# Optimization experiments

Measured on AMD Instinct MI355X. Metric: run time of the kernel, lower is better.

The kernel has to match this reference:

```python
import jax, jax.numpy as jnp
import numpy as np

B, C, H, W = 2, 64, 192, 192
K = 3
KK = K * K  # 9 kernel taps


def conv2d(x, w, b, dilation=1, padding=1):
    # NCHW / OIHW 3x3 conv, stride 1
    out = jax.lax.conv_general_dilated(
        x, w, window_strides=(1, 1),
        padding=[(padding, padding), (padding, padding)],
        rhs_dilation=(dilation, dilation),
        dimension_numbers=('NCHW', 'OIHW', 'NCHW'))
    return out + b[None, :, None, None]


def channel_ln(x, w, b, eps=1e-5):
    # WithBias_LayerNorm over the channel axis (to_3d puts C last)
    mu = jnp.mean(x, axis=1, keepdims=True)
    var = jnp.mean((x - mu) ** 2, axis=1, keepdims=True)  # biased var
    xn = (x - mu) / jnp.sqrt(var + eps)
    return xn * w[None, :, None, None] + b[None, :, None, None]


def mod_deform_conv(x, offset, mask, w, b):
    # Modulated deformable conv (mmcv semantics): stride 1, pad 1, dil 1,
    # deform_groups=1. offset: [B,2*KK,H,W] (dy,dx interleaved per tap),
    # mask: [B,KK,H,W].
    Bb, Cc, Hh, Ww = x.shape
    off = offset.reshape(Bb, KK, 2, Hh, Ww)
    kidx = jnp.arange(K)
    ky, kx = jnp.meshgrid(kidx, kidx, indexing='ij')
    ky = ky.reshape(KK).astype(x.dtype)
    kx = kx.reshape(KK).astype(x.dtype)
    hh = jnp.arange(Hh, dtype=x.dtype)
    ww = jnp.arange(Ww, dtype=x.dtype)
    # sample positions: out_pos - pad + tap + learned offset  -> [B,KK,H,W]
    py = off[:, :, 0] + hh[None, None, :, None] - 1.0 + ky[None, :, None, None]
    px = off[:, :, 1] + ww[None, None, None, :] - 1.0 + kx[None, :, None, None]
    y0f = jnp.floor(py)
    x0f = jnp.floor(px)
    ly = py - y0f
    lx = px - x0f
    y0 = y0f.astype(jnp.int32)
    x0 = x0f.astype(jnp.int32)
    xf = x.reshape(Bb, Cc, Hh * Ww)

    def corner(yi, xi, wgt):
        valid = (yi >= 0) & (yi < Hh) & (xi >= 0) & (xi < Ww)
        idx = (jnp.clip(yi, 0, Hh - 1) * Ww + jnp.clip(xi, 0, Ww - 1)).reshape(Bb, -1)
        g = jax.vmap(lambda xb, ib: xb[:, ib])(xf, idx)  # [B,C,KK*H*W]
        wv = (wgt * valid.astype(x.dtype)).reshape(Bb, 1, -1)
        return g * wv

    val = (corner(y0, x0, (1 - ly) * (1 - lx))
           + corner(y0, x0 + 1, (1 - ly) * lx)
           + corner(y0 + 1, x0, ly * (1 - lx))
           + corner(y0 + 1, x0 + 1, ly * lx))
    val = val.reshape(Bb, Cc, KK, Hh, Ww) * mask[:, None]  # modulate
    out = jnp.einsum('bckhw,ock->bohw', val, w.reshape(w.shape[0], Cc, KK))
    return out + b[None, :, None, None]


def setup_inputs() -> dict:
    key = jax.random.key(0)
    ks = jax.random.split(key, 8)
    x = jax.random.normal(ks[0], (B, C, H, W), jnp.float32)
    pre_mask = jax.random.uniform(ks[1], (B, 1, H, W), jnp.float32)
    ln_w = jnp.ones((C,), jnp.float32)
    ln_b = jnp.zeros((C,), jnp.float32)
    # offset/mask convs are zero-init in the original; use small random
    # weights so the bilinear gather is actually exercised (offsets ~ few px)
    off_w = jax.random.normal(ks[2], (2 * KK, C, 3, 3), jnp.float32) * 0.02
    off_b = jnp.zeros((2 * KK,), jnp.float32)
    mask_w = jax.random.normal(ks[3], (KK, C, 3, 3), jnp.float32) * 0.02
    mask_b = jnp.zeros((KK,), jnp.float32)
    scale = 1.0 / np.sqrt(C * KK)
    def_w = jax.random.normal(ks[4], (C, C, 3, 3), jnp.float32) * scale
    def_b = jnp.zeros((C,), jnp.float32)
    fus_w = jax.random.normal(ks[5], (C, C, 3, 3), jnp.float32) * scale
    fus_b = jnp.zeros((C,), jnp.float32)
    return {'x': x, 'pre_mask': pre_mask, 'ln_w': ln_w, 'ln_b': ln_b,
            'off_w': off_w, 'off_b': off_b, 'mask_w': mask_w, 'mask_b': mask_b,
            'def_w': def_w, 'def_b': def_b, 'fus_w': fus_w, 'fus_b': fus_b}


def reference(x, pre_mask, ln_w, ln_b, off_w, off_b, mask_w, mask_b,
              def_w, def_b, fus_w, fus_b):
    inp = x
    xn = channel_ln(x, ln_w, ln_b)
    # only the dilation=1 offset/mask branch feeds the single def_conv
    offset = conv2d(xn, off_w, off_b, dilation=1, padding=1)
    mask = jax.nn.sigmoid(conv2d(xn, mask_w, mask_b, dilation=1, padding=1))
    x_def = mod_deform_conv(xn, offset, mask, def_w, def_b)
    # single def_conv -> stack+sum is identity
    return conv2d(x_def, fus_w, fus_b) * pre_mask + inp * (1.0 - pre_mask)
```

## Files before the change

### kernel.cpp

```cpp
#include <hip/hip_runtime.h>
#include <hip/hip_bf16.h>
#include <math.h>

#define B_ 2
#define C_ 64
#define H_ 192
#define W_ 192
#define HW_ (H_*W_)
#define BHW_ (B_*HW_)
#define KK_ 9
#define CK_ (C_*KK_)
#define KSTEPS_ (CK_/32)
#define TX_ 12
#define WROWS_ 6
#define WCOLS_ 21
#define WCHUNKS_ (WROWS_*WCOLS_*8)
#define FWROWS_ 4
#define FWCOLS_ 18
#define FWCHUNKS_ (FWROWS_*FWCOLS_*8)

typedef __bf16 bf16x8 __attribute__((ext_vector_type(8)));
typedef float  f32x4  __attribute__((ext_vector_type(4)));
typedef unsigned short ushortx8 __attribute__((ext_vector_type(8)));
typedef unsigned short ushortx4 __attribute__((ext_vector_type(4)));

__device__ __forceinline__ float bf2f(unsigned short u) {
    unsigned int t = ((unsigned int)u) << 16;
    return __builtin_bit_cast(float, t);
}
__device__ __forceinline__ unsigned short f2bf(float f) {
    __hip_bfloat16 hb = __float2bfloat16(f);
    return *reinterpret_cast<unsigned short*>(&hb);
}

__global__ void ln_prepack_kernel(const float* __restrict__ x,
                                  const float* __restrict__ lnw,
                                  const float* __restrict__ lnb,
                                  unsigned short* __restrict__ xnb,
                                  const float* __restrict__ dw,
                                  const float* __restrict__ fw,
                                  const float* __restrict__ offw,
                                  const float* __restrict__ maskw,
                                  unsigned short* __restrict__ wpack,
                                  unsigned short* __restrict__ wpf,
                                  unsigned short* __restrict__ wpc) {
    if (blockIdx.x < 288) {
        int p = blockIdx.x * 256 + threadIdx.x;
        int b = p / HW_, pix = p % HW_;
        const float* xb = x + (size_t)b * C_ * HW_ + pix;
        float v[C_];
        float s = 0.f, s2 = 0.f;
        #pragma unroll
        for (int c = 0; c < C_; ++c) {
            v[c] = xb[(size_t)c * HW_];
            s += v[c]; s2 += v[c] * v[c];
        }
        float mu  = s * (1.0f / C_);
        float var = s2 * (1.0f / C_) - mu * mu;
        float inv = rsqrtf(var + 1e-5f);
        unsigned short* zb = xnb + (size_t)p * 64;
        #pragma unroll
        for (int g = 0; g < 8; ++g) {
            ushortx8 st;
            #pragma unroll
            for (int j = 0; j < 8; ++j) {
                int c = g * 8 + j;
                st[j] = f2bf((v[c] - mu) * inv * lnw[c] + lnb[c]);
            }
            *reinterpret_cast<ushortx8*>(zb + g * 8) = st;
        }
        return;
    }
    const int n1 = 4 * KSTEPS_ * 64 * 8;
    const int n2 = 4 * KSTEPS_ * 64 * 8;
    const int n3 = 2 * KSTEPS_ * 64 * 8;
    int gid = (blockIdx.x - 288) * 256 + threadIdx.x;
    int nth = 36 * 256;
    for (int idx = gid; idx < n1 + n2 + n3; idx += nth) {
        int which = (idx < n1) ? 0 : (idx < n1 + n2 ? 1 : 2);
        int rem = idx - (which == 0 ? 0 : (which == 1 ? n1 : n1 + n2));
        int j = rem & 7;
        int l = (rem >> 3) & 63;
        int rest = rem >> 9;
        int s = rest % KSTEPS_;
        int t = rest / KSTEPS_;
        int oc = t * 16 + (l & 15);
        int ck = s * 32 + (l >> 4) * 8 + j;
        int k = ck >> 6, c = ck & 63;
        float v;
        if (which == 0) {
            v = dw[(size_t)oc * CK_ + c * 9 + k];
        } else if (which == 1) {
            v = fw[(size_t)oc * CK_ + c * 9 + k];
        } else {
            v = (oc < 18) ? offw[(size_t)oc * CK_ + c * 9 + k]
              : (oc < 27) ? maskw[(size_t)(oc - 18) * CK_ + c * 9 + k]
              : 0.f;
        }
        unsigned short u = f2bf(v);
        if (which == 0) wpack[rem] = u;
        else if (which == 1) wpf[rem] = u;
        else wpc[rem] = u;
    }
}

__global__ void __launch_bounds__(128) dc_mfma(
        const unsigned short* __restrict__ xnb,
        const unsigned short* __restrict__ wpc,
        const float* __restrict__ offb, const float* __restrict__ maskb,
        const unsigned short* __restrict__ wpack,
        const float* __restrict__ db,
        unsigned short* __restrict__ xdefb) {
    __shared__ ushortx8 win[WCHUNKS_];
    __shared__ float som[32][36];
    int tid  = threadIdx.x;
    int wave = tid >> 6;
    int lane = tid & 63;
    int bid  = blockIdx.x;
    int rg   = bid % (H_ / 2);
    int rest = bid / (H_ / 2);
    int tx   = rest % TX_;
    int b    = rest / TX_;
    int pq = lane & 15;
    int kchunk = lane >> 4;
    int h0 = rg * 2;
    int w0 = tx * 16, w = w0 + pq;

    const unsigned short* xb = xnb + (size_t)b * HW_ * 64;

    #pragma unroll
    for (int i = 0; i < 8; ++i) {
        int idx = i * 128 + tid;
        if (idx < WCHUNKS_) {
            int r    = idx / (WCOLS_ * 8);
            int rem2 = idx - r * (WCOLS_ * 8);
            int c    = rem2 >> 3;
            int seg  = rem2 & 7;
            int gy = min(max(h0 - 2 + r, 0), H_ - 1);
            int gx = min(max(w0 - 2 + c, 0), W_ - 1);
            ushortx8 v = *reinterpret_cast<const ushortx8*>(
                xb + ((size_t)(gy * W_ + gx) * 64 + seg * 8));
            win[(r * WCOLS_ + c) * 8 + (seg ^ (c & 7))] = v;
        }
    }
    __syncthreads();

    f32x4 cacc[2][2];
    #pragma unroll
    for (int pg = 0; pg < 2; ++pg)
        #pragma unroll
        for (int t = 0; t < 2; ++t) cacc[pg][t] = f32x4{0.f, 0.f, 0.f, 0.f};

    #pragma unroll
    for (int s = 0; s < KSTEPS_; ++s) {
        const int k = s >> 1;
        const int dy = k / 3 - 1, dxk = k % 3 - 1;
        int wc = pq + dxk + 2;
        int sidx = ((s & 1) * 4 + kchunk) ^ (wc & 7);
        bf16x8 af[2];
        #pragma unroll
        for (int t = 0; t < 2; ++t)
            af[t] = *reinterpret_cast<const bf16x8*>(
                wpc + ((size_t)(t * KSTEPS_ + s) * 64 + lane) * 8);
        #pragma unroll
        for (int pg = 0; pg < 2; ++pg) {
            int hp = h0 + pg;
            bool ok = ((unsigned)(hp + dy) < (unsigned)H_) &&
                      ((unsigned)(w + dxk) < (unsigned)W_);
            int wr = pg + dy + 2;
            ushortx8 u = win[(wr * WCOLS_ + wc) * 8 + sidx];
            if (!ok) u = ushortx8{0, 0, 0, 0, 0, 0, 0, 0};
            bf16x8 bv = __builtin_bit_cast(bf16x8, u);
            #pragma unroll
            for (int t = 0; t < 2; ++t)
                cacc[pg][t] = __builtin_amdgcn_mfma_f32_16x16x32_bf16(af[t], bv, cacc[pg][t], 0, 0, 0);
        }
    }

    #pragma unroll
    for (int pg = 0; pg < 2; ++pg) {
        #pragma unroll
        for (int t = 0; t < 2; ++t) {
            f32x4 sv;
            #pragma unroll
            for (int r = 0; r < 4; ++r) {
                int oc = t * 16 + kchunk * 4 + r;
                float a = cacc[pg][t][r];
                if (oc < 18)      sv[r] = a + offb[oc];
                else if (oc < 27) sv[r] = 1.f / (1.f + expf(-(a + maskb[oc - 18])));
                else              sv[r] = 0.f;
            }
            *reinterpret_cast<f32x4*>(&som[pg * 16 + pq][t * 16 + kchunk * 4]) = sv;
        }
    }

    f32x4 acc[2][4];
    #pragma unroll
    for (int pg = 0; pg < 2; ++pg)
        #pragma unroll
        for (int t = 0; t < 4; ++t) acc[pg][t] = f32x4{0.f, 0.f, 0.f, 0.f};

    auto tapbody = [&](int k) {
        #pragma unroll
        for (int pg = 0; pg < 2; ++pg) {
            int hp = h0 + pg;
            const float* om = som[pg * 16 + pq];
            float dy = om[2 * k], dx = om[2 * k + 1], m = om[18 + k];
            float py = dy + (float)(hp - 1 + k / 3);
            float px = dx + (float)(w - 1 + k % 3);
            float fy = floorf(py), fx = floorf(px);
            float ly = py - fy, lx = px - fx;
            int y0 = (int)fy, x0 = (int)fx;
            int y1 = y0 + 1, x1 = x0 + 1;
            bool oky0 = (unsigned)y0 < (unsigned)H_;
            bool oky1 = (unsigned)y1 < (unsigned)H_;
            bool okx0 = (unsigned)x0 < (unsigned)W_;
            bool okx1 = (unsigned)x1 < (unsigned)W_;
            float q[4];
            q[0] = (oky0 && okx0) ? (1.f - ly) * (1.f - lx) * m : 0.f;
            q[1] = (oky0 && okx1) ? (1.f - ly) * lx * m : 0.f;
            q[2] = (oky1 && okx0) ? ly * (1.f - lx) * m : 0.f;
            q[3] = (oky1 && okx1) ? ly * lx * m : 0.f;
            int wr0 = y0 - (h0 - 2), wr1 = y1 - (h0 - 2);
            int wc0 = x0 - (w0 - 2), wc1 = x1 - (w0 - 2);
            bool inr0 = (unsigned)wr0 < (unsigned)WROWS_;
            bool inr1 = (unsigned)wr1 < (unsigned)WROWS_;
            bool inc0 = (unsigned)wc0 < (unsigned)WCOLS_;
            bool inc1 = (unsigned)wc1 < (unsigned)WCOLS_;
            bool in[4];
            in[0] = inr0 && inc0; in[1] = inr0 && inc1;
            in[2] = inr1 && inc0; in[3] = inr1 && inc1;
            int swr0 = min(max(wr0, 0), WROWS_ - 1), swr1 = min(max(wr1, 0), WROWS_ - 1);
            int swc0 = min(max(wc0, 0), WCOLS_ - 1), swc1 = min(max(wc1, 0), WCOLS_ - 1);
            int cb[4], sx[4];
            cb[0] = (swr0 * WCOLS_ + swc0) * 8; sx[0] = swc0 & 7;
            cb[1] = (swr0 * WCOLS_ + swc1) * 8; sx[1] = swc1 & 7;
            cb[2] = (swr1 * WCOLS_ + swc0) * 8; sx[2] = swc0 & 7;
            cb[3] = (swr1 * WCOLS_ + swc1) * 8; sx[3] = swc1 & 7;
            int cy0 = min(max(y0, 0), H_ - 1), cy1 = min(max(y1, 0), H_ - 1);
            int cx0 = min(max(x0, 0), W_ - 1), cx1 = min(max(x1, 0), W_ - 1);
            int ga[4];
            ga[0] = cy0 * W_ + cx0; ga[1] = cy0 * W_ + cx1;
            ga[2] = cy1 * W_ + cx0; ga[3] = cy1 * W_ + cx1;

            #pragma unroll
            for (int half = 0; half < 2; ++half) {
                int s = k * 2 + half;
                int seg = half * 4 + kchunk;
                int cbg = half * 32 + kchunk * 8;
                ushortx8 v[4];
                #pragma unroll
                for (int c = 0; c < 4; ++c) v[c] = win[cb[c] + (seg ^ sx[c])];
                #pragma unroll
                for (int c = 0; c < 4; ++c)
                    if (q[c] != 0.f && !in[c])
                        v[c] = *reinterpret_cast<const ushortx8*>(
                            xb + ((size_t)ga[c] * 64 + cbg));
                union { unsigned short u[8]; bf16x8 v; } bu;
                #pragma unroll
                for (int j = 0; j < 8; ++j) {
                    float a = q[0] * bf2f(v[0][j]) + q[1] * bf2f(v[1][j])
                            + q[2] * bf2f(v[2][j]) + q[3] * bf2f(v[3][j]);
                    bu.u[j] = f2bf(a);
                }
                #pragma unroll
                for (int t = 0; t < 4; ++t) {
                    bf16x8 afr = *reinterpret_cast<const bf16x8*>(
                        wpack + ((size_t)(t * KSTEPS_ + s) * 64 + lane) * 8);
                    acc[pg][t] = __builtin_amdgcn_mfma_f32_16x16x32_bf16(
                        afr, bu.v, acc[pg][t], 0, 0, 0);
                }
            }
        }
    };

    if (wave == 0) {
        tapbody(0); tapbody(1); tapbody(2); tapbody(3);
    } else {
        tapbody(4); tapbody(5); tapbody(6); tapbody(7); tapbody(8);
    }

    __syncthreads();
    float* red = reinterpret_cast<float*>(win);
    {
        float* slot = red + (wave * 64 + lane) * 17;
        if (wave == 0) {
            #pragma unroll
            for (int t = 0; t < 4; ++t)
                #pragma unroll
                for (int r = 0; r < 4; ++r) slot[t * 4 + r] = acc[1][t][r];
        } else {
            #pragma unroll
            for (int t = 0; t < 4; ++t)
                #pragma unroll
                for (int r = 0; r < 4; ++r) slot[t * 4 + r] = acc[0][t][r];
        }
    }
    __syncthreads();
    {
        const float* pslot = red + ((1 - wave) * 64 + lane) * 17;
        int hp = h0 + wave;
        unsigned short* zb = xdefb + ((size_t)(b * HW_ + hp * W_ + w)) * 64;
        if (wave == 0) {
            #pragma unroll
            for (int t = 0; t < 4; ++t) {
                ushortx4 st;
                #pragma unroll
                for (int r = 0; r < 4; ++r) {
                    int oc = t * 16 + kchunk * 4 + r;
                    st[r] = f2bf(acc[0][t][r] + pslot[t * 4 + r] + db[oc]);
                }
                *reinterpret_cast<ushortx4*>(zb + t * 16 + kchunk * 4) = st;
            }
        } else {
            #pragma unroll
            for (int t = 0; t < 4; ++t) {
                ushortx4 st;
                #pragma unroll
                for (int r = 0; r < 4; ++r) {
                    int oc = t * 16 + kchunk * 4 + r;
                    st[r] = f2bf(acc[1][t][r] + pslot[t * 4 + r] + db[oc]);
                }
                *reinterpret_cast<ushortx4*>(zb + t * 16 + kchunk * 4) = st;
            }
        }
    }
}

__global__ void __launch_bounds__(128) fuse_mfma(
        const unsigned short* __restrict__ xdefb,
        const unsigned short* __restrict__ wpf,
        const float* __restrict__ fb,
        const float* __restrict__ premask,
        const float* __restrict__ xin,
        float* __restrict__ out) {
    __shared__ ushortx8 fwin[FWCHUNKS_];
    int tid  = threadIdx.x;
    int wave = tid >> 6;
    int lane = tid & 63;
    int bid  = blockIdx.x;
    int rg   = bid % (H_ / 2);
    int rest = bid / (H_ / 2);
    int tx   = rest % TX_;
    int b    = rest / TX_;
    int pq = lane & 15;
    int kchunk = lane >> 4;
    int h0 = rg * 2;
    int w0 = tx * 16, w = w0 + pq;

    const unsigned short* xb = xdefb + (size_t)b * HW_ * 64;

    #pragma unroll
    for (int i = 0; i < 5; ++i) {
        int idx = i * 128 + tid;
        if (idx < FWCHUNKS_) {
            int r    = idx / (FWCOLS_ * 8);
            int rem2 = idx - r * (FWCOLS_ * 8);
            int c    = rem2 >> 3;
            int seg  = rem2 & 7;
            int gy = min(max(h0 - 1 + r, 0), H_ - 1);
            int gx = min(max(w0 - 1 + c, 0), W_ - 1);
            ushortx8 v = *reinterpret_cast<const ushortx8*>(
                xb + ((size_t)(gy * W_ + gx) * 64 + seg * 8));
            fwin[(r * FWCOLS_ + c) * 8 + (seg ^ (c & 7))] = v;
        }
    }
    __syncthreads();

    f32x4 acc[2][4];
    #pragma unroll
    for (int pg = 0; pg < 2; ++pg)
        #pragma unroll
        for (int t = 0; t < 4; ++t) acc[pg][t] = f32x4{0.f, 0.f, 0.f, 0.f};

    auto stepbody = [&](int s) {
        const int k = s >> 1;
        const int dy = k / 3 - 1, dxk = k % 3 - 1;
        int wc = pq + dxk + 1;
        int sidx = ((s & 1) * 4 + kchunk) ^ (wc & 7);
        bf16x8 af[4];
        #pragma unroll
        for (int t = 0; t < 4; ++t)
            af[t] = *reinterpret_cast<const bf16x8*>(
                wpf + ((size_t)(t * KSTEPS_ + s) * 64 + lane) * 8);
        #pragma unroll
        for (int pg = 0; pg < 2; ++pg) {
            int hp = h0 + pg;
            bool ok = ((unsigned)(hp + dy) < (unsigned)H_) &&
                      ((unsigned)(w + dxk) < (unsigned)W_);
            int wr = pg + dy + 1;
            ushortx8 u = fwin[(wr * FWCOLS_ + wc) * 8 + sidx];
            if (!ok) u = ushortx8{0, 0, 0, 0, 0, 0, 0, 0};
            bf16x8 bv = __builtin_bit_cast(bf16x8, u);
            #pragma unroll
            for (int t = 0; t < 4; ++t)
                acc[pg][t] = __builtin_amdgcn_mfma_f32_16x16x32_bf16(af[t], bv, acc[pg][t], 0, 0, 0);
        }
    };

    if (wave == 0) {
        stepbody(0); stepbody(1); stepbody(2); stepbody(3); stepbody(4);
        stepbody(5); stepbody(6); stepbody(7); stepbody(8);
    } else {
        stepbody(9); stepbody(10); stepbody(11); stepbody(12); stepbody(13);
        stepbody(14); stepbody(15); stepbody(16); stepbody(17);
    }

    __syncthreads();
    float* red = reinterpret_cast<float*>(fwin);
    {
        float* slot = red + (wave * 64 + lane) * 17;
        if (wave == 0) {
            #pragma unroll
            for (int t = 0; t < 4; ++t)
                #pragma unroll
                for (int r = 0; r < 4; ++r) slot[t * 4 + r] = acc[1][t][r];
        } else {
            #pragma unroll
            for (int t = 0; t < 4; ++t)
                #pragma unroll
                for (int r = 0; r < 4; ++r) slot[t * 4 + r] = acc[0][t][r];
        }
    }
    __syncthreads();
    {
        const float* pslot = red + ((1 - wave) * 64 + lane) * 17;
        int hp = h0 + wave;
        int pix = hp * W_ + w;
        float pm = premask[(size_t)b * HW_ + pix];
        if (wave == 0) {
            #pragma unroll
            for (int t = 0; t < 4; ++t) {
                #pragma unroll
                for (int r = 0; r < 4; ++r) {
                    int oc = t * 16 + kchunk * 4 + r;
                    size_t oidx = ((size_t)b * C_ + oc) * HW_ + pix;
                    float a = acc[0][t][r] + pslot[t * 4 + r] + fb[oc];
                    out[oidx] = a * pm + xin[oidx] * (1.f - pm);
                }
            }
        } else {
            #pragma unroll
            for (int t = 0; t < 4; ++t) {
                #pragma unroll
                for (int r = 0; r < 4; ++r) {
                    int oc = t * 16 + kchunk * 4 + r;
                    size_t oidx = ((size_t)b * C_ + oc) * HW_ + pix;
                    float a = acc[1][t][r] + pslot[t * 4 + r] + fb[oc];
                    out[oidx] = a * pm + xin[oidx] * (1.f - pm);
                }
            }
        }
    }
}

extern "C" void kernel_launch(void* const* d_in, const int* in_sizes, int n_in,
                              void* d_out, int out_size, void* d_ws, size_t ws_size,
                              hipStream_t stream) {
    const float* x       = (const float*)d_in[0];
    const float* premask = (const float*)d_in[1];
    const float* lnw     = (const float*)d_in[2];
    const float* lnb     = (const float*)d_in[3];
    const float* offw    = (const float*)d_in[4];
    const float* offb    = (const float*)d_in[5];
    const float* maskw   = (const float*)d_in[6];
    const float* maskb   = (const float*)d_in[7];
    const float* dw      = (const float*)d_in[8];
    const float* db      = (const float*)d_in[9];
    const float* fw      = (const float*)d_in[10];
    const float* fb      = (const float*)d_in[11];
    float* out = (float*)d_out;

    char* ws = (char*)d_ws;
    unsigned short* xnb   = (unsigned short*)ws;  ws += sizeof(short) * (size_t)BHW_ * 64;
    unsigned short* xdefb = (unsigned short*)ws;  ws += sizeof(short) * (size_t)BHW_ * 64;
    unsigned short* wpack = (unsigned short*)ws;  ws += sizeof(short) * 4 * KSTEPS_ * 64 * 8;
    unsigned short* wpf   = (unsigned short*)ws;  ws += sizeof(short) * 4 * KSTEPS_ * 64 * 8;
    unsigned short* wpc   = (unsigned short*)ws;  ws += sizeof(short) * 2 * KSTEPS_ * 64 * 8;

    const int grid = B_ * TX_ * (H_ / 2);

    ln_prepack_kernel<<<288 + 36, 256, 0, stream>>>(
        x, lnw, lnb, xnb, dw, fw, offw, maskw, wpack, wpf, wpc);
    dc_mfma<<<grid, 128, 0, stream>>>(
        xnb, wpc, offb, maskb, wpack, db, xdefb);
    fuse_mfma<<<grid, 128, 0, stream>>>(xdefb, wpf, fb, premask, x, out);
}
```

Baseline: 74.97 us.

## Split offset conv rows across waves and software-pipeline deform tap gathers

The offset/mask conv stage is now split so each of the two waves computes one output row instead of both waves computing both rows redundantly, followed by a barrier before the deform stage reads the shared offset table. The deform tap loop is restructured into prep (coordinate math plus LDS/global corner loads) and blend (bilinear mix plus MFMA) phases, double-buffered so the next tap's loads are issued before the current tap's math. This is meant to hide LDS and global gather latency and remove duplicated MFMA work, at the cost of more live registers (two sets of eight vector buffers) and an extra block barrier.

```diff
diff --git a/kernel.cpp b/kernel.cpp
--- a/kernel.cpp
+++ b/kernel.cpp
@@ -145,54 +145,45 @@
     }
     __syncthreads();
 
-    f32x4 cacc[2][2];
-    #pragma unroll
-    for (int pg = 0; pg < 2; ++pg)
-        #pragma unroll
-        for (int t = 0; t < 2; ++t) cacc[pg][t] = f32x4{0.f, 0.f, 0.f, 0.f};
-
-    #pragma unroll
-    for (int s = 0; s < KSTEPS_; ++s) {
-        const int k = s >> 1;
-        const int dy = k / 3 - 1, dxk = k % 3 - 1;
-        int wc = pq + dxk + 2;
-        int sidx = ((s & 1) * 4 + kchunk) ^ (wc & 7);
-        bf16x8 af[2];
-        #pragma unroll
-        for (int t = 0; t < 2; ++t)
-            af[t] = *reinterpret_cast<const bf16x8*>(
-                wpc + ((size_t)(t * KSTEPS_ + s) * 64 + lane) * 8);
-        #pragma unroll
-        for (int pg = 0; pg < 2; ++pg) {
-            int hp = h0 + pg;
+    {
+        int hp = h0 + wave;
+        f32x4 cacc[2];
+        cacc[0] = f32x4{0.f, 0.f, 0.f, 0.f};
+        cacc[1] = f32x4{0.f, 0.f, 0.f, 0.f};
+        #pragma unroll
+        for (int s = 0; s < KSTEPS_; ++s) {
+            const int k = s >> 1;
+            const int dy = k / 3 - 1, dxk = k % 3 - 1;
+            int wc = pq + dxk + 2;
+            int sidx = ((s & 1) * 4 + kchunk) ^ (wc & 7);
             bool ok = ((unsigned)(hp + dy) < (unsigned)H_) &&
                       ((unsigned)(w + dxk) < (unsigned)W_);
-            int wr = pg + dy + 2;
+            int wr = wave + dy + 2;
             ushortx8 u = win[(wr * WCOLS_ + wc) * 8 + sidx];
             if (!ok) u = ushortx8{0, 0, 0, 0, 0, 0, 0, 0};
             bf16x8 bv = __builtin_bit_cast(bf16x8, u);
             #pragma unroll
-            for (int t = 0; t < 2; ++t)
-                cacc[pg][t] = __builtin_amdgcn_mfma_f32_16x16x32_bf16(af[t], bv, cacc[pg][t], 0, 0, 0);
-        }
-    }
-
-    #pragma unroll
-    for (int pg = 0; pg < 2; ++pg) {
+            for (int t = 0; t < 2; ++t) {
+                bf16x8 afrag = *reinterpret_cast<const bf16x8*>(
+                    wpc + ((size_t)(t * KSTEPS_ + s) * 64 + lane) * 8);
+                cacc[t] = __builtin_amdgcn_mfma_f32_16x16x32_bf16(afrag, bv, cacc[t], 0, 0, 0);
+            }
+        }
         #pragma unroll
         for (int t = 0; t < 2; ++t) {
             f32x4 sv;
             #pragma unroll
             for (int r = 0; r < 4; ++r) {
                 int oc = t * 16 + kchunk * 4 + r;
-                float a = cacc[pg][t][r];
+                float a = cacc[t][r];
                 if (oc < 18)      sv[r] = a + offb[oc];
                 else if (oc < 27) sv[r] = 1.f / (1.f + expf(-(a + maskb[oc - 18])));
                 else              sv[r] = 0.f;
             }
-            *reinterpret_cast<f32x4*>(&som[pg * 16 + pq][t * 16 + kchunk * 4]) = sv;
-        }
-    }
+            *reinterpret_cast<f32x4*>(&som[wave * 16 + pq][t * 16 + kchunk * 4]) = sv;
+        }
+    }
+    __syncthreads();
 
     f32x4 acc[2][4];
     #pragma unroll
@@ -200,84 +191,108 @@
         #pragma unroll
         for (int t = 0; t < 4; ++t) acc[pg][t] = f32x4{0.f, 0.f, 0.f, 0.f};
 
-    auto tapbody = [&](int k) {
-        #pragma unroll
-        for (int pg = 0; pg < 2; ++pg) {
-            int hp = h0 + pg;
-            const float* om = som[pg * 16 + pq];
-            float dy = om[2 * k], dx = om[2 * k + 1], m = om[18 + k];
-            float py = dy + (float)(hp - 1 + k / 3);
-            float px = dx + (float)(w - 1 + k % 3);
-            float fy = floorf(py), fx = floorf(px);
-            float ly = py - fy, lx = px - fx;
-            int y0 = (int)fy, x0 = (int)fx;
-            int y1 = y0 + 1, x1 = x0 + 1;
-            bool oky0 = (unsigned)y0 < (unsigned)H_;
-            bool oky1 = (unsigned)y1 < (unsigned)H_;
-            bool okx0 = (unsigned)x0 < (unsigned)W_;
-            bool okx1 = (unsigned)x1 < (unsigned)W_;
-            float q[4];
-            q[0] = (oky0 && okx0) ? (1.f - ly) * (1.f - lx) * m : 0.f;
-            q[1] = (oky0 && okx1) ? (1.f - ly) * lx * m : 0.f;
-            q[2] = (oky1 && okx0) ? ly * (1.f - lx) * m : 0.f;
-            q[3] = (oky1 && okx1) ? ly * lx * m : 0.f;
-            int wr0 = y0 - (h0 - 2), wr1 = y1 - (h0 - 2);
-            int wc0 = x0 - (w0 - 2), wc1 = x1 - (w0 - 2);
-            bool inr0 = (unsigned)wr0 < (unsigned)WROWS_;
-            bool inr1 = (unsigned)wr1 < (unsigned)WROWS_;
-            bool inc0 = (unsigned)wc0 < (unsigned)WCOLS_;
-            bool inc1 = (unsigned)wc1 < (unsigned)WCOLS_;
-            bool in[4];
-            in[0] = inr0 && inc0; in[1] = inr0 && inc1;
-            in[2] = inr1 && inc0; in[3] = inr1 && inc1;
-            int swr0 = min(max(wr0, 0), WROWS_ - 1), swr1 = min(max(wr1, 0), WROWS_ - 1);
-            int swc0 = min(max(wc0, 0), WCOLS_ - 1), swc1 = min(max(wc1, 0), WCOLS_ - 1);
-            int cb[4], sx[4];
-            cb[0] = (swr0 * WCOLS_ + swc0) * 8; sx[0] = swc0 & 7;
-            cb[1] = (swr0 * WCOLS_ + swc1) * 8; sx[1] = swc1 & 7;
-            cb[2] = (swr1 * WCOLS_ + swc0) * 8; sx[2] = swc0 & 7;
-            cb[3] = (swr1 * WCOLS_ + swc1) * 8; sx[3] = swc1 & 7;
-            int cy0 = min(max(y0, 0), H_ - 1), cy1 = min(max(y1, 0), H_ - 1);
-            int cx0 = min(max(x0, 0), W_ - 1), cx1 = min(max(x1, 0), W_ - 1);
-            int ga[4];
-            ga[0] = cy0 * W_ + cx0; ga[1] = cy0 * W_ + cx1;
-            ga[2] = cy1 * W_ + cx0; ga[3] = cy1 * W_ + cx1;
-
-            #pragma unroll
-            for (int half = 0; half < 2; ++half) {
-                int s = k * 2 + half;
-                int seg = half * 4 + kchunk;
-                int cbg = half * 32 + kchunk * 8;
-                ushortx8 v[4];
-                #pragma unroll
-                for (int c = 0; c < 4; ++c) v[c] = win[cb[c] + (seg ^ sx[c])];
-                #pragma unroll
-                for (int c = 0; c < 4; ++c)
-                    if (q[c] != 0.f && !in[c])
-                        v[c] = *reinterpret_cast<const ushortx8*>(
-                            xb + ((size_t)ga[c] * 64 + cbg));
-                union { unsigned short u[8]; bf16x8 v; } bu;
-                #pragma unroll
-                for (int j = 0; j < 8; ++j) {
-                    float a = q[0] * bf2f(v[0][j]) + q[1] * bf2f(v[1][j])
-                            + q[2] * bf2f(v[2][j]) + q[3] * bf2f(v[3][j]);
-                    bu.u[j] = f2bf(a);
-                }
-                #pragma unroll
-                for (int t = 0; t < 4; ++t) {
-                    bf16x8 afr = *reinterpret_cast<const bf16x8*>(
-                        wpack + ((size_t)(t * KSTEPS_ + s) * 64 + lane) * 8);
-                    acc[pg][t] = __builtin_amdgcn_mfma_f32_16x16x32_bf16(
-                        afr, bu.v, acc[pg][t], 0, 0, 0);
-                }
+    float    qA[4], qB[4];
+    ushortx8 vA[8], vB[8];
+
+    auto prep = [&](int pg, int k, float* q, ushortx8* vb) {
+        int hp = h0 + pg;
+        const float* om = som[pg * 16 + pq];
+        float dy = om[2 * k], dx = om[2 * k + 1], m = om[18 + k];
+        float py = dy + (float)(hp - 1 + k / 3);
+        float px = dx + (float)(w - 1 + k % 3);
+        float fy = floorf(py), fx = floorf(px);
+        float ly = py - fy, lx = px - fx;
+        int y0 = (int)fy, x0 = (int)fx;
+        int y1 = y0 + 1, x1 = x0 + 1;
+        bool oky0 = (unsigned)y0 < (unsigned)H_;
+        bool oky1 = (unsigned)y1 < (unsigned)H_;
+        bool okx0 = (unsigned)x0 < (unsigned)W_;
+        bool okx1 = (unsigned)x1 < (unsigned)W_;
+        q[0] = (oky0 && okx0) ? (1.f - ly) * (1.f - lx) * m : 0.f;
+        q[1] = (oky0 && okx1) ? (1.f - ly) * lx * m : 0.f;
+        q[2] = (oky1 && okx0) ? ly * (1.f - lx) * m : 0.f;
+        q[3] = (oky1 && okx1) ? ly * lx * m : 0.f;
+        int wr0 = y0 - (h0 - 2), wr1 = y1 - (h0 - 2);
+        int wc0 = x0 - (w0 - 2), wc1 = x1 - (w0 - 2);
+        bool inr0 = (unsigned)wr0 < (unsigned)WROWS_;
+        bool inr1 = (unsigned)wr1 < (unsigned)WROWS_;
+        bool inc0 = (unsigned)wc0 < (unsigned)WCOLS_;
+        bool inc1 = (unsigned)wc1 < (unsigned)WCOLS_;
+        bool in[4];
+        in[0] = inr0 && inc0; in[1] = inr0 && inc1;
+        in[2] = inr1 && inc0; in[3] = inr1 && inc1;
+        int swr0 = min(max(wr0, 0), WROWS_ - 1), swr1 = min(max(wr1, 0), WROWS_ - 1);
+        int swc0 = min(max(wc0, 0), WCOLS_ - 1), swc1 = min(max(wc1, 0), WCOLS_ - 1);
+        int cb[4], sx[4];
+        cb[0] = (swr0 * WCOLS_ + swc0) * 8; sx[0] = swc0 & 7;
+        cb[1] = (swr0 * WCOLS_ + swc1) * 8; sx[1] = swc1 & 7;
+        cb[2] = (swr1 * WCOLS_ + swc0) * 8; sx[2] = swc0 & 7;
+        cb[3] = (swr1 * WCOLS_ + swc1) * 8; sx[3] = swc1 & 7;
+        int cy0 = min(max(y0, 0), H_ - 1), cy1 = min(max(y1, 0), H_ - 1);
+        int cx0 = min(max(x0, 0), W_ - 1), cx1 = min(max(x1, 0), W_ - 1);
+        int ga[4];
+        ga[0] = cy0 * W_ + cx0; ga[1] = cy0 * W_ + cx1;
+        ga[2] = cy1 * W_ + cx0; ga[3] = cy1 * W_ + cx1;
+        #pragma unroll
+        for (int half = 0; half < 2; ++half) {
+            int seg = half * 4 + kchunk;
+            int cbg = half * 32 + kchunk * 8;
+            #pragma unroll
+            for (int c = 0; c < 4; ++c) {
+                ushortx8 v = win[cb[c] + (seg ^ sx[c])];
+                if (q[c] != 0.f && !in[c])
+                    v = *reinterpret_cast<const ushortx8*>(
+                        xb + ((size_t)ga[c] * 64 + cbg));
+                vb[half * 4 + c] = v;
             }
         }
     };
 
+    auto blend = [&](int pg, int k, const float* q, const ushortx8* vb) {
+        #pragma unroll
+        for (int half = 0; half < 2; ++half) {
+            int s = k * 2 + half;
+            union { unsigned short u[8]; bf16x8 v; } bu;
+            #pragma unroll
+            for (int j = 0; j < 8; ++j) {
+                float a = q[0] * bf2f(vb[half * 4 + 0][j])
+                        + q[1] * bf2f(vb[half * 4 + 1][j])
+                        + q[2] * bf2f(vb[half * 4 + 2][j])
+                        + q[3] * bf2f(vb[half * 4 + 3][j]);
+                bu.u[j] = f2bf(a);
+            }
+            #pragma unroll
+            for (int t = 0; t < 4; ++t) {
+                bf16x8 afr = *reinterpret_cast<const bf16x8*>(
+                    wpack + ((size_t)(t * KSTEPS_ + s) * 64 + lane) * 8);
+                acc[pg][t] = __builtin_amdgcn_mfma_f32_16x16x32_bf16(
+                    afr, bu.v, acc[pg][t], 0, 0, 0);
+            }
+        }
+    };
+
     if (wave == 0) {
-        tapbody(0); tapbody(1); tapbody(2); tapbody(3);
+        prep(0, 0, qA, vA);
+        prep(0, 1, qB, vB); blend(0, 0, qA, vA);
+        prep(0, 2, qA, vA); blend(0, 1, qB, vB);
+        prep(0, 3, qB, vB); blend(0, 2, qA, vA);
+        prep(1, 0, qA, vA); blend(0, 3, qB, vB);
+        prep(1, 1, qB, vB); blend(1, 0, qA, vA);
+        prep(1, 2, qA, vA); blend(1, 1, qB, vB);
+        prep(1, 3, qB, vB); blend(1, 2, qA, vA);
+        blend(1, 3, qB, vB);
     } else {
-        tapbody(4); tapbody(5); tapbody(6); tapbody(7); tapbody(8);
+        prep(0, 4, qA, vA);
+        prep(0, 5, qB, vB); blend(0, 4, qA, vA);
+        prep(0, 6, qA, vA); blend(0, 5, qB, vB);
+        prep(0, 7, qB, vB); blend(0, 6, qA, vA);
+        prep(0, 8, qA, vA); blend(0, 7, qB, vB);
+        prep(1, 4, qB, vB); blend(0, 8, qA, vA);
+        prep(1, 5, qA, vA); blend(1, 4, qB, vB);
+        prep(1, 6, qB, vB); blend(1, 5, qA, vA);
+        prep(1, 7, qA, vA); blend(1, 6, qB, vB);
+        prep(1, 8, qB, vB); blend(1, 7, qA, vA);
+        blend(1, 8, qB, vB);
     }
 
     __syncthreads();
```

Measured after the change: 94.82 us. 26.5% more time.
